# Kernel optimization log

Hardware: AMD Instinct MI355X
Metric: run time of the kernel (lower is better)

Reference implementation:

```python
import jax, jax.numpy as jnp
import numpy as np


def setup_inputs() -> dict:
    key = jax.random.key(0)
    ks = jax.random.split(key, 9)
    B, C, H, W, E = 8, 128, 64, 64, 64
    s = 0.05
    return {
        "feature": jax.random.normal(ks[0], (B, C, H, W), jnp.float32),
        "w_q": jax.random.normal(ks[1], (E, C), jnp.float32) * s,
        "b_q": jax.random.normal(ks[2], (E,), jnp.float32) * s,
        "w_k": jax.random.normal(ks[3], (E, C), jnp.float32) * s,
        "b_k": jax.random.normal(ks[4], (E,), jnp.float32) * s,
        "w_v": jax.random.normal(ks[5], (E, C), jnp.float32) * s,
        "b_v": jax.random.normal(ks[6], (E,), jnp.float32) * s,
        "w_att": jax.random.normal(ks[7], (C, E), jnp.float32) * s,
        "b_att": jax.random.normal(ks[8], (C,), jnp.float32) * s,
    }


def reference(feature, w_q, b_q, w_k, b_k, w_v, b_v, w_att, b_att):
    B, C, H, W = feature.shape
    E = w_q.shape[0]
    x = feature.reshape(B, C, H * W)  # (B, C, N) -- 1x1 conv == channel GEMM
    q = jnp.einsum("ec,bcn->ben", w_q, x) + b_q[None, :, None]
    k = jnp.einsum("ec,bcn->ben", w_k, x) + b_k[None, :, None]
    v = jnp.einsum("ec,bcn->ben", w_v, x) + b_v[None, :, None]
    # att[b,i,j] = sum_e K[b,e,i] * Q[b,e,j]; softmax over j (torch dim=2)
    att = jnp.einsum("bei,bej->bij", k, q)
    att = jax.nn.softmax(att, axis=-1)
    # out[b,e,j] = sum_i V[b,e,i] * att[b,i,j]  (torch matmul(value, att))
    fgs = jnp.einsum("bei,bij->bej", v, att)
    out = jnp.einsum("ce,ben->bcn", w_att, fgs) + b_att[None, :, None]
    return out.reshape(B, C, H, W)
```

## Files before the change

kernel.cpp:

```cpp
#include <hip/hip_runtime.h>
#include <hip/hip_bf16.h>
#include <string.h>


#define LOG2E 1.4426950408889634f

typedef short bfrag __attribute__((ext_vector_type(8)));
typedef float f32x16 __attribute__((ext_vector_type(16)));

#define MFMA(a, b, c) __builtin_amdgcn_mfma_f32_32x32x16_bf16(a, b, c, 0, 0, 0)

__device__ __forceinline__ short f2bf(float f) {
  __hip_bfloat16 h = __float2bfloat16(f);
  short s;
  __builtin_memcpy(&s, &h, 2);
  return s;
}
__device__ __forceinline__ float bf2f(short s) {
  unsigned u = ((unsigned)(unsigned short)s) << 16;
  float f;
  __builtin_memcpy(&f, &u, 4);
  return f;
}
__device__ __forceinline__ f32x16 zero16() {
  f32x16 z;
#pragma unroll
  for (int r = 0; r < 16; ++r) z[r] = 0.f;
  return z;
}

__global__ void k_pack(const float* __restrict__ wq, const float* __restrict__ wk,
                       const float* __restrict__ wv, const float* __restrict__ watt,
                       short* __restrict__ WF, short* __restrict__ WattF) {
  int idx = blockIdx.x * 256 + threadIdx.x;
  if (idx < 24576) {
    int t = idx & 7, l = (idx >> 3) & 63, kg = (idx >> 9) & 7, mt = idx >> 12;
    int e = mt * 32 + (l & 31);
    int c = 16 * kg + 4 * (l >> 5) + (t & 3) + 8 * (t >> 2);
    const float* src = (e < 64) ? wq : ((e < 128) ? wk : wv);
    WF[idx] = f2bf(src[(e & 63) * 128 + c]);
  } else {
    int i2 = idx - 24576;
    int t = i2 & 7, l = (i2 >> 3) & 63, kg = (i2 >> 9) & 3, mt = i2 >> 11;
    int cr = mt * 32 + (l & 31);
    int e = 16 * kg + 4 * (l >> 5) + (t & 3) + 8 * (t >> 2);
    WattF[i2] = f2bf(watt[cr * 64 + e]);
  }
}

__global__ __launch_bounds__(256) void k_qkv(
    const float* __restrict__ feat, const short* __restrict__ WF,
    const float* __restrict__ bq, const float* __restrict__ bk, const float* __restrict__ bv,
    short* __restrict__ Qf, short* __restrict__ Kf, short* __restrict__ Vf) {
  __shared__ short xf[16384];
  int jb = blockIdx.x, b = blockIdx.y;
  int tid = threadIdx.x;
  int p0 = jb * 128;
  for (int idx = tid; idx < 16384; idx += 256) {
    int c = idx >> 7, pl = idx & 127;
    float v = feat[((b * 128 + c) << 12) + p0 + pl];
    int tt = pl >> 5, pn = pl & 31;
    int kg = c >> 4, cw = c & 15;
    int l = pn + 32 * ((cw >> 2) & 1);
    int t = (cw & 3) + 4 * (cw >> 3);
    xf[((tt * 8 + kg) * 64 + l) * 8 + t] = f2bf(v);
  }
  __syncthreads();
  int w = tid >> 6, lane = tid & 63;
  int jt = jb * 4 + w;
  bfrag xr[8];
#pragma unroll
  for (int kg = 0; kg < 8; ++kg)
    xr[kg] = *(const bfrag*)&xf[((w * 8 + kg) * 64 + lane) * 8];
  int el[16];
#pragma unroll
  for (int r = 0; r < 16; ++r) el[r] = (r & 3) + 8 * (r >> 2) + 4 * (lane >> 5);

#pragma unroll
  for (int mt = 0; mt < 6; ++mt) {
    f32x16 acc = zero16();
#pragma unroll
    for (int kg = 0; kg < 8; ++kg) {
      bfrag wf = *(const bfrag*)&WF[((mt * 8 + kg) * 64 + lane) * 8];
      if (mt < 4) acc = MFMA(wf, xr[kg], acc);
      else        acc = MFMA(xr[kg], wf, acc);
    }
    bfrag o0, o1;
    if (mt < 2) {
#pragma unroll
      for (int r = 0; r < 8; ++r) {
        o0[r] = f2bf(acc[r] + bq[mt * 32 + el[r]]);
        o1[r] = f2bf(acc[r + 8] + bq[mt * 32 + el[r + 8]]);
      }
      short* base = Qf + (((b * 128 + jt) * 4 + 2 * mt) * 64 + lane) * 8;
      *(bfrag*)base = o0;
      *(bfrag*)(base + 512) = o1;
    } else if (mt < 4) {
#pragma unroll
      for (int r = 0; r < 8; ++r) {
        o0[r] = f2bf((acc[r] + bk[(mt - 2) * 32 + el[r]]) * LOG2E);
        o1[r] = f2bf((acc[r + 8] + bk[(mt - 2) * 32 + el[r + 8]]) * LOG2E);
      }
      short* base = Kf + (((b * 128 + jt) * 4 + 2 * (mt - 2)) * 64 + lane) * 8;
      *(bfrag*)base = o0;
      *(bfrag*)(base + 512) = o1;
    } else {
      float bias = bv[(mt - 4) * 32 + (lane & 31)];
#pragma unroll
      for (int r = 0; r < 8; ++r) {
        o0[r] = f2bf(acc[r] + bias);
        o1[r] = f2bf(acc[r + 8] + bias);
      }
      short* base = Vf + (((b * 2 + (mt - 4)) * 256 + 2 * jt) * 64 + lane) * 8;
      *(bfrag*)base = o0;
      *(bfrag*)(base + 512) = o1;
    }
  }
}

__global__ __launch_bounds__(256) void k_pass1(
    const short* __restrict__ Kf, const short* __restrict__ Qf,
    float* __restrict__ sumsP) {
  __shared__ int4 ldsQ[256];
  int ib = blockIdx.x, b = blockIdx.y, jc = blockIdx.z;
  int tid = threadIdx.x, w = tid >> 6, lane = tid & 63;
  int it = ib * 4 + w;
  bfrag kf[4];
#pragma unroll
  for (int kg = 0; kg < 4; ++kg)
    kf[kg] = *(const bfrag*)&Kf[(((b * 128 + it) * 4 + kg) * 64 + lane) * 8];
  float part[16];
#pragma unroll
  for (int r = 0; r < 16; ++r) part[r] = 0.f;

  for (int s = 0; s < 32; ++s) {
    int jt = jc * 32 + s;
    const int4* qsrc = (const int4*)(Qf + (size_t)(b * 128 + jt) * 2048);
    int4 v = qsrc[tid];
    __syncthreads();
    ldsQ[tid] = v;
    __syncthreads();
    f32x16 acc = zero16();
#pragma unroll
    for (int kg = 0; kg < 4; ++kg) {
      bfrag qf = *(const bfrag*)&ldsQ[kg * 64 + lane];
      acc = MFMA(kf[kg], qf, acc);
    }
#pragma unroll
    for (int r = 0; r < 16; ++r) part[r] += __builtin_amdgcn_exp2f(acc[r]);
  }
#pragma unroll
  for (int r = 0; r < 16; ++r) {
    float v = part[r];
#pragma unroll
    for (int m = 1; m < 32; m <<= 1) v += __shfl_xor(v, m, 64);
    part[r] = v;
  }
  if ((lane & 31) == 0) {
    int h = lane >> 5;
#pragma unroll
    for (int r = 0; r < 16; ++r) {
      int i = it * 32 + (r & 3) + 8 * (r >> 2) + 4 * h;
      sumsP[(b * 4096 + i) * 4 + jc] = part[r];
    }
  }
}

__global__ void k_finl(const float* __restrict__ sumsP, float* __restrict__ invl) {
  int idx = blockIdx.x * 256 + threadIdx.x;
  const float* s = sumsP + (size_t)idx * 4;
  invl[idx] = 1.0f / (s[0] + s[1] + s[2] + s[3]);
}

__global__ void k_scalev(short* __restrict__ Vf, const float* __restrict__ invl) {
  int lin = blockIdx.x * 256 + threadIdx.x;
  int l = lin & 63, ig = (lin >> 6) & 255, b = lin >> 15;
  short* p = Vf + (size_t)lin * 8;
  bfrag v = *(const bfrag*)p;
  bfrag o;
#pragma unroll
  for (int t = 0; t < 8; ++t) {
    int i = 16 * ig + 4 * (l >> 5) + (t & 3) + 8 * (t >> 2);
    o[t] = f2bf(bf2f(v[t]) * invl[b * 4096 + i]);
  }
  *(bfrag*)p = o;
}

__global__ __launch_bounds__(256) void k_pass2(
    const short* __restrict__ Qf, const short* __restrict__ Kf, const short* __restrict__ Vf,
    float* __restrict__ fgsP) {
  __shared__ int4 ldsKV[512];
  int jb = blockIdx.x, b = blockIdx.y, ic = blockIdx.z;
  int tid = threadIdx.x, w = tid >> 6, lane = tid & 63;
  int jt = jb * 4 + w;
  bfrag qf[4];
#pragma unroll
  for (int kg = 0; kg < 4; ++kg)
    qf[kg] = *(const bfrag*)&Qf[(((b * 128 + jt) * 4 + kg) * 64 + lane) * 8];
  f32x16 f0 = zero16(), f1 = zero16();

  for (int s = 0; s < 32; ++s) {
    int it = ic * 32 + s;
    const int4* ksrc = (const int4*)(Kf + (size_t)(b * 128 + it) * 2048);
    int4 r0 = ksrc[tid];
    const int4* vsrc0 = (const int4*)(Vf + ((size_t)(b * 2 + 0) * 256 + 2 * it) * 512);
    const int4* vsrc1 = (const int4*)(Vf + ((size_t)(b * 2 + 1) * 256 + 2 * it) * 512);
    int4 r1 = (tid < 128) ? vsrc0[tid] : vsrc1[tid - 128];
    __syncthreads();
    ldsKV[tid] = r0;
    ldsKV[256 + tid] = r1;
    __syncthreads();
    f32x16 sacc = zero16();
#pragma unroll
    for (int kg = 0; kg < 4; ++kg) {
      bfrag kfr = *(const bfrag*)&ldsKV[kg * 64 + lane];
      sacc = MFMA(kfr, qf[kg], sacc);
    }
    bfrag pb0, pb1;
#pragma unroll
    for (int t = 0; t < 8; ++t) {
      pb0[t] = f2bf(__builtin_amdgcn_exp2f(sacc[t]));
      pb1[t] = f2bf(__builtin_amdgcn_exp2f(sacc[t + 8]));
    }
    bfrag v00 = *(const bfrag*)&ldsKV[256 + 0 * 64 + lane];
    bfrag v01 = *(const bfrag*)&ldsKV[256 + 1 * 64 + lane];
    bfrag v10 = *(const bfrag*)&ldsKV[256 + 2 * 64 + lane];
    bfrag v11 = *(const bfrag*)&ldsKV[256 + 3 * 64 + lane];
    f0 = MFMA(v00, pb0, f0);
    f0 = MFMA(v01, pb1, f0);
    f1 = MFMA(v10, pb0, f1);
    f1 = MFMA(v11, pb1, f1);
  }
  size_t obase = ((size_t)(ic * 8 + b) * 128 + jt) * 4;
#pragma unroll
  for (int h = 0; h < 2; ++h) {
    float* d0 = fgsP + ((obase + 0 + h) * 64 + lane) * 8;
    float* d1 = fgsP + ((obase + 2 + h) * 64 + lane) * 8;
#pragma unroll
    for (int t = 0; t < 8; ++t) {
      d0[t] = f0[8 * h + t];
      d1[t] = f1[8 * h + t];
    }
  }
}

__global__ void k_comb(const float* __restrict__ fgsP, short* __restrict__ fgsF) {
  int idx = blockIdx.x * 256 + threadIdx.x;
  const float* s = fgsP + (size_t)idx * 8;
  bfrag o;
#pragma unroll
  for (int t = 0; t < 8; ++t) {
    float v = s[t] + s[t + 2097152] + s[t + 2 * 2097152] + s[t + 3 * 2097152];
    o[t] = f2bf(v);
  }
  *(bfrag*)(fgsF + (size_t)idx * 8) = o;
}

__global__ __launch_bounds__(256) void k_out(
    const short* __restrict__ fgsF, const short* __restrict__ WattF,
    const float* __restrict__ batt, float* __restrict__ out) {
  int jb = blockIdx.x, b = blockIdx.y;
  int tid = threadIdx.x, w = tid >> 6, lane = tid & 63;
  int jt = jb * 4 + w;
  bfrag gf[4];
#pragma unroll
  for (int kg = 0; kg < 4; ++kg)
    gf[kg] = *(const bfrag*)&fgsF[(((b * 128 + jt) * 4 + kg) * 64 + lane) * 8];
  int n = jt * 32 + (lane & 31);
#pragma unroll
  for (int mt = 0; mt < 4; ++mt) {
    f32x16 acc = zero16();
#pragma unroll
    for (int kg = 0; kg < 4; ++kg) {
      bfrag wf = *(const bfrag*)&WattF[((mt * 4 + kg) * 64 + lane) * 8];
      acc = MFMA(wf, gf[kg], acc);
    }
#pragma unroll
    for (int r = 0; r < 16; ++r) {
      int c = 32 * mt + (r & 3) + 8 * (r >> 2) + 4 * (lane >> 5);
      out[((size_t)(b * 128 + c) << 12) + n] = acc[r] + batt[c];
    }
  }
}

extern "C" void kernel_launch(void* const* d_in, const int* in_sizes, int n_in,
                              void* d_out, int out_size, void* d_ws, size_t ws_size,
                              hipStream_t stream) {
  const float* feat = (const float*)d_in[0];
  const float* wq = (const float*)d_in[1];
  const float* bq = (const float*)d_in[2];
  const float* wk = (const float*)d_in[3];
  const float* bk = (const float*)d_in[4];
  const float* wv = (const float*)d_in[5];
  const float* bv = (const float*)d_in[6];
  const float* watt = (const float*)d_in[7];
  const float* batt = (const float*)d_in[8];
  float* out = (float*)d_out;

  char* ws = (char*)d_ws;
  short* WF = (short*)(ws);
  short* WattF = (short*)(ws + 49152);
  short* Qf = (short*)(ws + 65536);
  short* Kf = (short*)(ws + 65536 + 4194304);
  short* Vf = (short*)(ws + 65536 + 2 * 4194304);
  float* sumsP = (float*)(ws + 65536 + 3 * 4194304);
  float* invl = (float*)(ws + 65536 + 3 * 4194304 + 524288);
  float* fgsP = (float*)(ws + 65536 + 3 * 4194304 + 524288 + 131072);
  short* fgsF = (short*)(ws + 65536 + 3 * 4194304 + 524288 + 131072 + 33554432);

  hipLaunchKernelGGL(k_pack, dim3(128), dim3(256), 0, stream, wq, wk, wv, watt, WF, WattF);
  hipLaunchKernelGGL(k_qkv, dim3(32, 8), dim3(256), 0, stream, feat, WF, bq, bk, bv, Qf, Kf, Vf);
  hipLaunchKernelGGL(k_pass1, dim3(32, 8, 4), dim3(256), 0, stream, Kf, Qf, sumsP);
  hipLaunchKernelGGL(k_finl, dim3(128), dim3(256), 0, stream, sumsP, invl);
  hipLaunchKernelGGL(k_scalev, dim3(1024), dim3(256), 0, stream, Vf, invl);
  hipLaunchKernelGGL(k_pass2, dim3(32, 8, 4), dim3(256), 0, stream, Qf, Kf, Vf, fgsP);
  hipLaunchKernelGGL(k_comb, dim3(1024), dim3(256), 0, stream, fgsP, fgsF);
  hipLaunchKernelGGL(k_out, dim3(32, 8), dim3(256), 0, stream, fgsF, WattF, batt, out);
}
```

Measured before the change: 119.1 us.

## Double-buffer LDS tiles in attention passes and fold partial-sum combine into output GEMM

k_pass1 and k_pass2 now use two LDS buffers and prefetch the next Q or K/V tile into registers while the current tile is computed. This cuts the per-iteration barriers from two to one and hides global load latency behind the MFMAs. The separate k_comb kernel is removed, and k_out sums the four fp32 partials from fgsP itself before converting to bf16. That saves one launch and a bf16 intermediate round trip, at the cost of doubled LDS use and more registers for the prefetch. MFMA accumulators now start from a hoisted zero vector.

After: 111.9 us. 1.06x faster.

```diff
diff --git a/kernel.cpp b/kernel.cpp
--- a/kernel.cpp
+++ b/kernel.cpp
@@ -68,6 +68,7 @@
   __syncthreads();
   int w = tid >> 6, lane = tid & 63;
   int jt = jb * 4 + w;
+  f32x16 z = zero16();
   bfrag xr[8];
 #pragma unroll
   for (int kg = 0; kg < 8; ++kg)
@@ -78,9 +79,10 @@
 
 #pragma unroll
   for (int mt = 0; mt < 6; ++mt) {
-    f32x16 acc = zero16();
-#pragma unroll
-    for (int kg = 0; kg < 8; ++kg) {
+    bfrag w0 = *(const bfrag*)&WF[((mt * 8 + 0) * 64 + lane) * 8];
+    f32x16 acc = (mt < 4) ? MFMA(w0, xr[0], z) : MFMA(xr[0], w0, z);
+#pragma unroll
+    for (int kg = 1; kg < 8; ++kg) {
       bfrag wf = *(const bfrag*)&WF[((mt * 8 + kg) * 64 + lane) * 8];
       if (mt < 4) acc = MFMA(wf, xr[kg], acc);
       else        acc = MFMA(xr[kg], wf, acc);
@@ -121,10 +123,11 @@
 __global__ __launch_bounds__(256) void k_pass1(
     const short* __restrict__ Kf, const short* __restrict__ Qf,
     float* __restrict__ sumsP) {
-  __shared__ int4 ldsQ[256];
+  __shared__ int4 ldsQ[2][256];
   int ib = blockIdx.x, b = blockIdx.y, jc = blockIdx.z;
   int tid = threadIdx.x, w = tid >> 6, lane = tid & 63;
   int it = ib * 4 + w;
+  f32x16 z = zero16();
   bfrag kf[4];
 #pragma unroll
   for (int kg = 0; kg < 4; ++kg)
@@ -133,21 +136,31 @@
 #pragma unroll
   for (int r = 0; r < 16; ++r) part[r] = 0.f;
 
+  int jt0 = jc * 32;
+  const int4* q0p = (const int4*)(Qf + (size_t)(b * 128 + jt0) * 2048);
+  int4 qc = q0p[tid];
+  ldsQ[0][tid] = qc;
+  int4 qn = ((const int4*)(Qf + (size_t)(b * 128 + jt0 + 1) * 2048))[tid];
+  __syncthreads();
+
   for (int s = 0; s < 32; ++s) {
-    int jt = jc * 32 + s;
-    const int4* qsrc = (const int4*)(Qf + (size_t)(b * 128 + jt) * 2048);
-    int4 v = qsrc[tid];
-    __syncthreads();
-    ldsQ[tid] = v;
-    __syncthreads();
-    f32x16 acc = zero16();
-#pragma unroll
-    for (int kg = 0; kg < 4; ++kg) {
-      bfrag qf = *(const bfrag*)&ldsQ[kg * 64 + lane];
-      acc = MFMA(kf[kg], qf, acc);
-    }
+    int cur = s & 1;
+    bfrag q0 = *(const bfrag*)&ldsQ[cur][0 * 64 + lane];
+    bfrag q1 = *(const bfrag*)&ldsQ[cur][1 * 64 + lane];
+    bfrag q2 = *(const bfrag*)&ldsQ[cur][2 * 64 + lane];
+    bfrag q3 = *(const bfrag*)&ldsQ[cur][3 * 64 + lane];
+    f32x16 acc = MFMA(kf[0], q0, z);
+    acc = MFMA(kf[1], q1, acc);
+    acc = MFMA(kf[2], q2, acc);
+    acc = MFMA(kf[3], q3, acc);
 #pragma unroll
     for (int r = 0; r < 16; ++r) part[r] += __builtin_amdgcn_exp2f(acc[r]);
+    if (s < 31) {
+      ldsQ[cur ^ 1][tid] = qn;
+      if (s < 30)
+        qn = ((const int4*)(Qf + (size_t)(b * 128 + jt0 + s + 2) * 2048))[tid];
+      __syncthreads();
+    }
   }
 #pragma unroll
   for (int r = 0; r < 16; ++r) {
@@ -189,47 +202,61 @@
 __global__ __launch_bounds__(256) void k_pass2(
     const short* __restrict__ Qf, const short* __restrict__ Kf, const short* __restrict__ Vf,
     float* __restrict__ fgsP) {
-  __shared__ int4 ldsKV[512];
+  __shared__ int4 lds[2][512];
   int jb = blockIdx.x, b = blockIdx.y, ic = blockIdx.z;
   int tid = threadIdx.x, w = tid >> 6, lane = tid & 63;
   int jt = jb * 4 + w;
+  f32x16 z = zero16();
   bfrag qf[4];
 #pragma unroll
   for (int kg = 0; kg < 4; ++kg)
     qf[kg] = *(const bfrag*)&Qf[(((b * 128 + jt) * 4 + kg) * 64 + lane) * 8];
-  f32x16 f0 = zero16(), f1 = zero16();
+  f32x16 f0 = z, f1 = z;
+
+  int it0 = ic * 32;
+  int vh = tid >> 7;
+  int vtid = tid & 127;
+  int4 kc = ((const int4*)(Kf + (size_t)(b * 128 + it0) * 2048))[tid];
+  int4 vc = ((const int4*)(Vf + ((size_t)(b * 2 + vh) * 256 + 2 * it0) * 512))[vtid];
+  lds[0][tid] = kc;
+  lds[0][256 + tid] = vc;
+  int4 kn = ((const int4*)(Kf + (size_t)(b * 128 + it0 + 1) * 2048))[tid];
+  int4 vn = ((const int4*)(Vf + ((size_t)(b * 2 + vh) * 256 + 2 * (it0 + 1)) * 512))[vtid];
+  __syncthreads();
 
   for (int s = 0; s < 32; ++s) {
-    int it = ic * 32 + s;
-    const int4* ksrc = (const int4*)(Kf + (size_t)(b * 128 + it) * 2048);
-    int4 r0 = ksrc[tid];
-    const int4* vsrc0 = (const int4*)(Vf + ((size_t)(b * 2 + 0) * 256 + 2 * it) * 512);
-    const int4* vsrc1 = (const int4*)(Vf + ((size_t)(b * 2 + 1) * 256 + 2 * it) * 512);
-    int4 r1 = (tid < 128) ? vsrc0[tid] : vsrc1[tid - 128];
-    __syncthreads();
-    ldsKV[tid] = r0;
-    ldsKV[256 + tid] = r1;
-    __syncthreads();
-    f32x16 sacc = zero16();
-#pragma unroll
-    for (int kg = 0; kg < 4; ++kg) {
-      bfrag kfr = *(const bfrag*)&ldsKV[kg * 64 + lane];
-      sacc = MFMA(kfr, qf[kg], sacc);
-    }
+    int cur = s & 1;
+    bfrag k0 = *(const bfrag*)&lds[cur][0 * 64 + lane];
+    bfrag k1 = *(const bfrag*)&lds[cur][1 * 64 + lane];
+    bfrag k2 = *(const bfrag*)&lds[cur][2 * 64 + lane];
+    bfrag k3 = *(const bfrag*)&lds[cur][3 * 64 + lane];
+    f32x16 sacc = MFMA(k0, qf[0], z);
+    sacc = MFMA(k1, qf[1], sacc);
+    sacc = MFMA(k2, qf[2], sacc);
+    sacc = MFMA(k3, qf[3], sacc);
     bfrag pb0, pb1;
 #pragma unroll
     for (int t = 0; t < 8; ++t) {
       pb0[t] = f2bf(__builtin_amdgcn_exp2f(sacc[t]));
       pb1[t] = f2bf(__builtin_amdgcn_exp2f(sacc[t + 8]));
     }
-    bfrag v00 = *(const bfrag*)&ldsKV[256 + 0 * 64 + lane];
-    bfrag v01 = *(const bfrag*)&ldsKV[256 + 1 * 64 + lane];
-    bfrag v10 = *(const bfrag*)&ldsKV[256 + 2 * 64 + lane];
-    bfrag v11 = *(const bfrag*)&ldsKV[256 + 3 * 64 + lane];
+    bfrag v00 = *(const bfrag*)&lds[cur][256 + 0 * 64 + lane];
+    bfrag v01 = *(const bfrag*)&lds[cur][256 + 1 * 64 + lane];
+    bfrag v10 = *(const bfrag*)&lds[cur][256 + 2 * 64 + lane];
+    bfrag v11 = *(const bfrag*)&lds[cur][256 + 3 * 64 + lane];
     f0 = MFMA(v00, pb0, f0);
     f0 = MFMA(v01, pb1, f0);
     f1 = MFMA(v10, pb0, f1);
     f1 = MFMA(v11, pb1, f1);
+    if (s < 31) {
+      lds[cur ^ 1][tid] = kn;
+      lds[cur ^ 1][256 + tid] = vn;
+      if (s < 30) {
+        kn = ((const int4*)(Kf + (size_t)(b * 128 + it0 + s + 2) * 2048))[tid];
+        vn = ((const int4*)(Vf + ((size_t)(b * 2 + vh) * 256 + 2 * (it0 + s + 2)) * 512))[vtid];
+      }
+      __syncthreads();
+    }
   }
   size_t obase = ((size_t)(ic * 8 + b) * 128 + jt) * 4;
 #pragma unroll
@@ -244,34 +271,39 @@
   }
 }
 
-__global__ void k_comb(const float* __restrict__ fgsP, short* __restrict__ fgsF) {
-  int idx = blockIdx.x * 256 + threadIdx.x;
-  const float* s = fgsP + (size_t)idx * 8;
-  bfrag o;
-#pragma unroll
-  for (int t = 0; t < 8; ++t) {
-    float v = s[t] + s[t + 2097152] + s[t + 2 * 2097152] + s[t + 3 * 2097152];
-    o[t] = f2bf(v);
-  }
-  *(bfrag*)(fgsF + (size_t)idx * 8) = o;
-}
-
 __global__ __launch_bounds__(256) void k_out(
-    const short* __restrict__ fgsF, const short* __restrict__ WattF,
+    const float* __restrict__ fgsP, const short* __restrict__ WattF,
     const float* __restrict__ batt, float* __restrict__ out) {
   int jb = blockIdx.x, b = blockIdx.y;
   int tid = threadIdx.x, w = tid >> 6, lane = tid & 63;
   int jt = jb * 4 + w;
+  f32x16 z = zero16();
   bfrag gf[4];
 #pragma unroll
-  for (int kg = 0; kg < 4; ++kg)
-    gf[kg] = *(const bfrag*)&fgsF[(((b * 128 + jt) * 4 + kg) * 64 + lane) * 8];
+  for (int kg = 0; kg < 4; ++kg) {
+    float s8[8];
+#pragma unroll
+    for (int t = 0; t < 8; ++t) s8[t] = 0.f;
+#pragma unroll
+    for (int ic = 0; ic < 4; ++ic) {
+      const float* p = fgsP + ((((size_t)ic * 8 + b) * 128 + jt) * 4 + kg) * 512 + lane * 8;
+      float4 a0 = *(const float4*)p;
+      float4 a1 = *(const float4*)(p + 4);
+      s8[0] += a0.x; s8[1] += a0.y; s8[2] += a0.z; s8[3] += a0.w;
+      s8[4] += a1.x; s8[5] += a1.y; s8[6] += a1.z; s8[7] += a1.w;
+    }
+    bfrag g;
+#pragma unroll
+    for (int t = 0; t < 8; ++t) g[t] = f2bf(s8[t]);
+    gf[kg] = g;
+  }
   int n = jt * 32 + (lane & 31);
 #pragma unroll
   for (int mt = 0; mt < 4; ++mt) {
-    f32x16 acc = zero16();
-#pragma unroll
-    for (int kg = 0; kg < 4; ++kg) {
+    bfrag w0 = *(const bfrag*)&WattF[((mt * 4 + 0) * 64 + lane) * 8];
+    f32x16 acc = MFMA(w0, gf[0], z);
+#pragma unroll
+    for (int kg = 1; kg < 4; ++kg) {
       bfrag wf = *(const bfrag*)&WattF[((mt * 4 + kg) * 64 + lane) * 8];
       acc = MFMA(wf, gf[kg], acc);
     }
@@ -306,7 +338,6 @@
   float* sumsP = (float*)(ws + 65536 + 3 * 4194304);
   float* invl = (float*)(ws + 65536 + 3 * 4194304 + 524288);
   float* fgsP = (float*)(ws + 65536 + 3 * 4194304 + 524288 + 131072);
-  short* fgsF = (short*)(ws + 65536 + 3 * 4194304 + 524288 + 131072 + 33554432);
 
   hipLaunchKernelGGL(k_pack, dim3(128), dim3(256), 0, stream, wq, wk, wv, watt, WF, WattF);
   hipLaunchKernelGGL(k_qkv, dim3(32, 8), dim3(256), 0, stream, feat, WF, bq, bk, bv, Qf, Kf, Vf);
@@ -314,6 +345,5 @@
   hipLaunchKernelGGL(k_finl, dim3(128), dim3(256), 0, stream, sumsP, invl);
   hipLaunchKernelGGL(k_scalev, dim3(1024), dim3(256), 0, stream, Vf, invl);
   hipLaunchKernelGGL(k_pass2, dim3(32, 8, 4), dim3(256), 0, stream, Qf, Kf, Vf, fgsP);
-  hipLaunchKernelGGL(k_comb, dim3(1024), dim3(256), 0, stream, fgsP, fgsF);
-  hipLaunchKernelGGL(k_out, dim3(32, 8), dim3(256), 0, stream, fgsF, WattF, batt, out);
-}
+  hipLaunchKernelGGL(k_out, dim3(32, 8), dim3(256), 0, stream, fgsP, WattF, batt, out);
+}
```
